# Optimization experiments

Hardware: AMD Instinct MI355X
Metric: run time of the kernel (lower is better)

The kernel has to match this reference:

```python
import jax, jax.numpy as jnp
import numpy as np

N_NODES = 50000
N_EDGES = 800000
IN_FEATS = 128
H_FEATS = 32
HEADS = 4
OUT_FEATS = 32
OUT_HEADS = 1
NEG_SLOPE = 0.2


def setup_inputs() -> dict:
    key = jax.random.key(0)
    ks = jax.random.split(key, 20)
    s = 0.05
    return {
        "features": jax.random.normal(ks[0], (N_NODES, IN_FEATS), jnp.float32),
        "src": jax.random.randint(ks[1], (N_EDGES,), 0, N_NODES, jnp.int32),
        "dst": jax.random.randint(ks[2], (N_EDGES,), 0, N_NODES, jnp.int32),
        "Ws0": jax.random.normal(ks[3], (IN_FEATS, HEADS * H_FEATS), jnp.float32) * s,
        "bs0": jnp.zeros((HEADS * H_FEATS,), jnp.float32),
        "Wd0": jax.random.normal(ks[4], (IN_FEATS, HEADS * H_FEATS), jnp.float32) * s,
        "bd0": jnp.zeros((HEADS * H_FEATS,), jnp.float32),
        "a0": jax.random.normal(ks[5], (HEADS, H_FEATS), jnp.float32) * s,
        "Ws1": jax.random.normal(ks[6], (HEADS * H_FEATS, HEADS * H_FEATS), jnp.float32) * s,
        "bs1": jnp.zeros((HEADS * H_FEATS,), jnp.float32),
        "Wd1": jax.random.normal(ks[7], (HEADS * H_FEATS, HEADS * H_FEATS), jnp.float32) * s,
        "bd1": jnp.zeros((HEADS * H_FEATS,), jnp.float32),
        "a1": jax.random.normal(ks[8], (HEADS, H_FEATS), jnp.float32) * s,
        "Ws2": jax.random.normal(ks[9], (HEADS * H_FEATS, OUT_HEADS * OUT_FEATS), jnp.float32) * s,
        "bs2": jnp.zeros((OUT_HEADS * OUT_FEATS,), jnp.float32),
        "Wd2": jax.random.normal(ks[10], (HEADS * H_FEATS, OUT_HEADS * OUT_FEATS), jnp.float32) * s,
        "bd2": jnp.zeros((OUT_HEADS * OUT_FEATS,), jnp.float32),
        "a2": jax.random.normal(ks[11], (OUT_HEADS, OUT_FEATS), jnp.float32) * s,
    }


def gatv2_conv(x, src, dst, Ws, bs, Wd, bd, attn, n_nodes):
    """DGL GATv2Conv (share_weights=False, residual=False, no dropout)."""
    heads, f = attn.shape
    feat_src = (x @ Ws + bs).reshape(-1, heads, f)  # [N, H, F]
    feat_dst = (x @ Wd + bd).reshape(-1, heads, f)  # [N, H, F]
    # per-edge GATv2 score: LeakyReLU(Wsrc h_u + Wdst h_v) . a
    e = jax.nn.leaky_relu(feat_src[src] + feat_dst[dst], NEG_SLOPE)  # [E, H, F]
    logits = jnp.einsum("ehf,hf->eh", e, attn)  # [E, H]
    # edge softmax over incoming edges of each dst node
    m = jax.ops.segment_max(logits, dst, num_segments=n_nodes)  # [N, H]
    ex = jnp.exp(logits - m[dst])
    denom = jax.ops.segment_sum(ex, dst, num_segments=n_nodes)  # [N, H]
    alpha = ex / denom[dst]  # [E, H]
    # scatter-aggregate messages
    msg = feat_src[src] * alpha[..., None]  # [E, H, F]
    return jax.ops.segment_sum(msg, dst, num_segments=n_nodes)  # [N, H, F]


def reference(features, src, dst,
              Ws0, bs0, Wd0, bd0, a0,
              Ws1, bs1, Wd1, bd1, a1,
              Ws2, bs2, Wd2, bd2, a2):
    n = features.shape[0]
    h = gatv2_conv(features, src, dst, Ws0, bs0, Wd0, bd0, a0, n)
    h = jax.nn.relu(h.reshape(n, -1))
    h = gatv2_conv(h, src, dst, Ws1, bs1, Wd1, bd1, a1, n)
    h = jax.nn.relu(h.reshape(n, -1))
    h = gatv2_conv(h, src, dst, Ws2, bs2, Wd2, bd2, a2, n)
    return h.mean(axis=1)  # [N, OUT_FEATS]
```

## Files before the change

kernel.cpp:

```cpp
#include <hip/hip_runtime.h>

typedef __attribute__((ext_vector_type(8))) short bf16x8;
typedef __attribute__((ext_vector_type(4))) float f32x4;

#define LOG2E 1.4426950408889634f

#define BINSH 8
#define NBIN 196
#define CHUNK 4096
#define K4CAP 6144

__device__ __forceinline__ unsigned bf_rn(float f) {
    unsigned u = __float_as_uint(f);
    u += 0x7fffu + ((u >> 16) & 1u);
    return u >> 16;
}
__device__ __forceinline__ float bf_lo(unsigned u) { return __uint_as_float(u << 16); }
__device__ __forceinline__ float bf_hi(unsigned u) { return __uint_as_float(u & 0xffff0000u); }

template <int CTRL>
__device__ __forceinline__ float dpp_radd(float x) {
    int t = __builtin_amdgcn_update_dpp(0, __float_as_int(x), CTRL, 0xF, 0xF, true);
    return x + __int_as_float(t);
}
__device__ __forceinline__ float sum8(float p) {
    p = dpp_radd<0x141>(p);
    p = dpp_radd<0x1B>(p);
    p = dpp_radd<0xB1>(p);
    return p;
}
__device__ __forceinline__ float dpp_swap1(float x) {
    return __int_as_float(__builtin_amdgcn_update_dpp(0, __float_as_int(x), 0xB1, 0xF, 0xF, true));
}

__device__ __forceinline__ float fast_exp2(float x) {
#if __has_builtin(__builtin_amdgcn_exp2f)
    return __builtin_amdgcn_exp2f(x);
#else
    return __expf(x * 0.6931471805599453f);
#endif
}


__global__ __launch_bounds__(256) void bin_count(const int* __restrict__ dst,
                                                 int* __restrict__ binCnt, int e) {
    __shared__ int hist[NBIN];
    for (int t = threadIdx.x; t < NBIN; t += 256) hist[t] = 0;
    __syncthreads();
    int base = blockIdx.x * CHUNK;
    int cnt = min(CHUNK, e - base);
    for (int j = threadIdx.x; j < cnt; j += 256)
        atomicAdd(&hist[dst[base + j] >> BINSH], 1);
    __syncthreads();
    for (int t = threadIdx.x; t < NBIN; t += 256)
        if (hist[t]) atomicAdd(&binCnt[t], hist[t]);
}

__global__ void bin_scan(const int* __restrict__ binCnt, int* __restrict__ binBase,
                         int* __restrict__ binCur, int* __restrict__ rowp, int n, int e) {
    int t = threadIdx.x;
    int v = (t < NBIN) ? binCnt[t] : 0;
    int lane = t & 63, w = t >> 6;
    int incl = v;
    for (int off = 1; off < 64; off <<= 1) {
        int tt = __shfl_up(incl, off);
        if (lane >= off) incl += tt;
    }
    __shared__ int wsum[4];
    if (lane == 63) wsum[w] = incl;
    __syncthreads();
    int wpre = 0;
    for (int i = 0; i < w; ++i) wpre += wsum[i];
    int excl = wpre + incl - v;
    if (t < NBIN) { binBase[t] = excl; binCur[t] = excl; }
    if (t == 0) { binBase[NBIN] = e; rowp[n] = e; }
}

__global__ __launch_bounds__(256) void bin_scatter(
    const int* __restrict__ src, const int* __restrict__ dst,
    int* __restrict__ binCur, unsigned* __restrict__ ebin, int e) {
    __shared__ int hist[NBIN];
    __shared__ int seg[NBIN];
    __shared__ int gbase[NBIN];
    __shared__ unsigned pack[CHUNK];
    for (int t = threadIdx.x; t < NBIN; t += 256) hist[t] = 0;
    __syncthreads();
    int base = blockIdx.x * CHUNK;
    int cnt = min(CHUNK, e - base);

    int myb[CHUNK / 256], myr[CHUNK / 256];
    unsigned myw[CHUNK / 256];
    int nmine = 0;
    for (int j = threadIdx.x; j < cnt; j += 256) {
        int d = dst[base + j], s = src[base + j];
        int b = d >> BINSH, dl = d & ((1 << BINSH) - 1);
        int r = atomicAdd(&hist[b], 1);
        myb[nmine] = b; myr[nmine] = r;
        myw[nmine] = ((unsigned)b << 24) | ((unsigned)dl << 16) | (unsigned)s;
        ++nmine;
    }
    __syncthreads();
    if (threadIdx.x == 0) {
        int acc = 0;
        for (int b2 = 0; b2 < NBIN; ++b2) { seg[b2] = acc; acc += hist[b2]; }
    }
    __syncthreads();
    for (int k = 0; k < nmine; ++k)
        pack[seg[myb[k]] + myr[k]] = myw[k];
    __syncthreads();
    if (threadIdx.x < NBIN && hist[threadIdx.x])
        gbase[threadIdx.x] = atomicAdd(&binCur[threadIdx.x], hist[threadIdx.x]);
    __syncthreads();
    for (int j = threadIdx.x; j < cnt; j += 256) {
        unsigned wv = pack[j];
        int b = wv >> 24;
        ebin[gbase[b] + (j - seg[b])] = wv;
    }
}

__global__ __launch_bounds__(256) void csr_build(
    const unsigned* __restrict__ ebin, const int* __restrict__ binBase,
    int* __restrict__ rowp, int* __restrict__ csrc, int n) {
    __shared__ int hist[256];
    __shared__ int seg[256];
    __shared__ unsigned stage[K4CAP];
    int b = blockIdx.x;
    int e0 = binBase[b], e1 = binBase[b + 1];
    int n0 = b << BINSH;
    int nn = min(256, n - n0);
    for (int t = threadIdx.x; t < 256; t += 256) hist[t] = 0;
    __syncthreads();
    for (int i = e0 + threadIdx.x; i < e1; i += 256) {
        unsigned wv = ebin[i];
        atomicAdd(&hist[(wv >> 16) & 255], 1);
        int off = i - e0;
        if (off < K4CAP) stage[off] = wv;
    }
    __syncthreads();
    if (threadIdx.x < 64) {
        int l = threadIdx.x;
        int s = 0, loc[4];
#pragma unroll
        for (int k = 0; k < 4; ++k) { loc[k] = s; s += hist[l * 4 + k]; }
        int incl = s;
        for (int off = 1; off < 64; off <<= 1) {
            int tt = __shfl_up(incl, off);
            if (l >= off) incl += tt;
        }
        int excl = incl - s;
#pragma unroll
        for (int k = 0; k < 4; ++k) seg[l * 4 + k] = excl + loc[k];
    }
    __syncthreads();
    for (int t = threadIdx.x; t < nn; t += 256) rowp[n0 + t] = e0 + seg[t];
    for (int t = threadIdx.x; t < 256; t += 256) hist[t] = seg[t];
    __syncthreads();
    for (int i = e0 + threadIdx.x; i < e1; i += 256) {
        int off = i - e0;
        unsigned wv = (off < K4CAP) ? stage[off] : ebin[i];
        int dl = (wv >> 16) & 255;
        int pos = e0 + atomicAdd(&hist[dl], 1);
        csrc[pos] = (int)(wv & 0xFFFFu);
    }
}


__global__ void convert_feat(const float* __restrict__ x, unsigned short* __restrict__ o, int n4) {
    int i = blockIdx.x * blockDim.x + threadIdx.x;
    if (i < n4) {
        float4 v = *(const float4*)(x + (size_t)i * 4);
        ushort4 r;
        r.x = (unsigned short)bf_rn(v.x); r.y = (unsigned short)bf_rn(v.y);
        r.z = (unsigned short)bf_rn(v.z); r.w = (unsigned short)bf_rn(v.w);
        *(ushort4*)(o + (size_t)i * 4) = r;
    }
}

__global__ void transpose_all(
    const float* __restrict__ Ws0, const float* __restrict__ Wd0,
    const float* __restrict__ Ws1, const float* __restrict__ Wd1,
    const float* __restrict__ Ws2, const float* __restrict__ Wd2,
    unsigned short* __restrict__ wt0, unsigned short* __restrict__ wt1,
    unsigned short* __restrict__ wt2) {
    int gid = blockIdx.x * blockDim.x + threadIdx.x;
    if (gid < 65536) {
        int l = gid >> 15, loc = gid & 32767;
        int c = loc >> 7, k = loc & 127;
        const float* W = (c < 128) ? (l ? Ws1 : Ws0) : (l ? Wd1 : Wd0);
        int cc = c & 127;
        float v = W[(size_t)k * 128 + cc];
        (l ? wt1 : wt0)[loc] = (unsigned short)bf_rn(v);
    } else if (gid < 65536 + 8192) {
        int loc = gid - 65536;
        int c = loc >> 7, k = loc & 127;
        const float* W = (c < 32) ? Ws2 : Wd2;
        int cc = (c < 32) ? c : c - 32;
        float v = W[(size_t)k * 32 + cc];
        wt2[loc] = (unsigned short)bf_rn(v);
    }
}


template <int COLS2>
__global__ __launch_bounds__(256) void gemm_dual2(
    const unsigned short* __restrict__ xb, const unsigned short* __restrict__ wt,
    const float* __restrict__ bs, const float* __restrict__ bd,
    unsigned short* __restrict__ fs, unsigned short* __restrict__ fd,
    int n, int nch) {
    constexpr int C  = COLS2 / 2;
    constexpr int NC = COLS2 / 64;

    const int lane = threadIdx.x & 63;
    const int m = lane & 15, quad = lane >> 4;
    const int gwid = blockIdx.x * 4 + (threadIdx.x >> 6);
    const int nwaves = gridDim.x * 4;
    const int cs = gwid % NC;
    const int cstride = nwaves / NC;

    float biasv[4];
#pragma unroll
    for (int ct = 0; ct < 4; ++ct) {
        int col = cs * 64 + ct * 16 + m;
        biasv[ct] = (col < C) ? bs[col] : bd[col - C];
    }

    for (int chunk = gwid / NC; chunk < nch; chunk += cstride) {
        const size_t r0 = (size_t)chunk * 64;

        f32x4 acc[4][4];
#pragma unroll
        for (int rt = 0; rt < 4; ++rt)
#pragma unroll
            for (int ct = 0; ct < 4; ++ct) acc[rt][ct] = (f32x4){0.f, 0.f, 0.f, 0.f};

#pragma unroll
        for (int ks = 0; ks < 4; ++ks) {
            const int ko = ks * 32 + quad * 8;
            bf16x8 a[4], b[4];
#pragma unroll
            for (int rt = 0; rt < 4; ++rt)
                a[rt] = *(const bf16x8*)(xb + (r0 + rt * 16 + m) * 128 + ko);
#pragma unroll
            for (int ct = 0; ct < 4; ++ct)
                b[ct] = *(const bf16x8*)(wt + (size_t)(cs * 64 + ct * 16 + m) * 128 + ko);
#pragma unroll
            for (int rt = 0; rt < 4; ++rt)
#pragma unroll
                for (int ct = 0; ct < 4; ++ct)
                    acc[rt][ct] = __builtin_amdgcn_mfma_f32_16x16x32_bf16(a[rt], b[ct], acc[rt][ct], 0, 0, 0);
        }

        const int odd = m & 1;
#pragma unroll
        for (int ct = 0; ct < 4; ++ct) {
            int colE = cs * 64 + ct * 16 + (m & ~1);
            unsigned short* ptr = (colE < C) ? fs : fd;
            int cc = (colE < C) ? colE : colE - C;
#pragma unroll
            for (int rt = 0; rt < 4; ++rt) {
                float v0 = acc[rt][ct][0] + biasv[ct];
                float v1 = acc[rt][ct][1] + biasv[ct];
                float v2 = acc[rt][ct][2] + biasv[ct];
                float v3 = acc[rt][ct][3] + biasv[ct];
                float s0 = dpp_swap1(v0), s1 = dpp_swap1(v1);
                float s2 = dpp_swap1(v2), s3 = dpp_swap1(v3);
                float aLo = odd ? s2 : v0, aHi = odd ? v2 : s0;
                float bLo = odd ? s3 : v1, bHi = odd ? v3 : s1;
                int rowA = (int)r0 + rt * 16 + quad * 4 + (odd ? 2 : 0);
                unsigned pa = (bf_rn(aHi) << 16) | bf_rn(aLo);
                unsigned pb = (bf_rn(bHi) << 16) | bf_rn(bLo);
                if (rowA < n)     *(unsigned*)(ptr + (size_t)rowA * C + cc)       = pa;
                if (rowA + 1 < n) *(unsigned*)(ptr + ((size_t)rowA + 1) * C + cc) = pb;
            }
        }
    }
}


#define EDGE_BODY(u, mval)                                          \
    do {                                                            \
        float x0 = bf_lo((u).x), x1 = bf_hi((u).x);                 \
        float x2 = bf_lo((u).y), x3 = bf_hi((u).y);                 \
        float t0 = x0 + fd0, t1 = x1 + fd1;                         \
        float t2 = x2 + fd2, t3 = x3 + fd3;                         \
        float p = a060 * t0;                                        \
        p = fmaf(a040, fabsf(t0), p);                               \
        p = fmaf(a061, t1, p); p = fmaf(a041, fabsf(t1), p);        \
        p = fmaf(a062, t2, p); p = fmaf(a042, fabsf(t2), p);        \
        p = fmaf(a063, t3, p); p = fmaf(a043, fabsf(t3), p);        \
        p = sum8(p);                                                \
        float ex = fast_exp2(p) * (mval);                           \
        denom += ex;                                                \
        acc0 = fmaf(ex, x0, acc0); acc1 = fmaf(ex, x1, acc1);       \
        acc2 = fmaf(ex, x2, acc2); acc3 = fmaf(ex, x3, acc3);       \
    } while (0)

__global__ __launch_bounds__(256) void conv128(
    const unsigned short* __restrict__ fs, const unsigned short* __restrict__ fd,
    const float* __restrict__ attn, const int* __restrict__ rowp,
    const int* __restrict__ csrc, unsigned short* __restrict__ out, int n) {
    const int nwaves = gridDim.x * 4;
    const int wid0 = blockIdx.x * 4 + (threadIdx.x >> 6);
    const int lane = threadIdx.x & 63;
    const int half = lane >> 5;
    const int q = lane & 31;

    float4 av = *(const float4*)(attn + q * 4);
    const float a060 = av.x * 0.6f * LOG2E, a040 = av.x * 0.4f * LOG2E;
    const float a061 = av.y * 0.6f * LOG2E, a041 = av.y * 0.4f * LOG2E;
    const float a062 = av.z * 0.6f * LOG2E, a042 = av.z * 0.4f * LOG2E;
    const float a063 = av.w * 0.6f * LOG2E, a043 = av.w * 0.4f * LOG2E;

    for (int wid = wid0; wid < n; wid += nwaves) {
        uint2 ud = *(const uint2*)(fd + (size_t)wid * 128 + q * 4);
        float fd0 = bf_lo(ud.x), fd1 = bf_hi(ud.x);
        float fd2 = bf_lo(ud.y), fd3 = bf_hi(ud.y);
        int rs = rowp[wid], re = rowp[wid + 1];
        float acc0 = 0.f, acc1 = 0.f, acc2 = 0.f, acc3 = 0.f, denom = 0.f;

        int i = rs;
        for (; i + 3 < re; i += 4) {
            int sA = csrc[i + half];
            int sB = csrc[i + 2 + half];
            uint2 uA = *(const uint2*)(fs + ((size_t)sA << 7) + q * 4);
            uint2 uB = *(const uint2*)(fs + ((size_t)sB << 7) + q * 4);
            EDGE_BODY(uA, 1.0f);
            EDGE_BODY(uB, 1.0f);
        }
        for (; i + 1 < re; i += 2) {
            int s = csrc[i + half];
            uint2 u = *(const uint2*)(fs + ((size_t)s << 7) + q * 4);
            EDGE_BODY(u, 1.0f);
        }
        if (i < re) {
            int s = csrc[i];
            uint2 u = *(const uint2*)(fs + ((size_t)s << 7) + q * 4);
            float mval = half ? 0.f : 1.f;
            EDGE_BODY(u, mval);
        }
        acc0 += __shfl_xor(acc0, 32); acc1 += __shfl_xor(acc1, 32);
        acc2 += __shfl_xor(acc2, 32); acc3 += __shfl_xor(acc3, 32);
        denom += __shfl_xor(denom, 32);
        float inv = (re > rs) ? 1.f / denom : 0.f;
        float r0 = fmaxf(acc0 * inv, 0.f), r1 = fmaxf(acc1 * inv, 0.f);
        float r2 = fmaxf(acc2 * inv, 0.f), r3 = fmaxf(acc3 * inv, 0.f);
        if (half == 0) {
            uint2 o;
            o.x = (bf_rn(r1) << 16) | bf_rn(r0);
            o.y = (bf_rn(r3) << 16) | bf_rn(r2);
            ((uint2*)(out + (size_t)wid * 128))[q] = o;
        }
    }
}

__global__ __launch_bounds__(256) void conv32(
    const unsigned short* __restrict__ fs, const unsigned short* __restrict__ fd,
    const float* __restrict__ attn, const int* __restrict__ rowp,
    const int* __restrict__ csrc, float* __restrict__ out, int n) {
    const int nwaves = gridDim.x * 4;
    const int wid0 = blockIdx.x * 4 + (threadIdx.x >> 6);
    const int lane = threadIdx.x & 63;
    const int g = lane >> 3;
    const int c = lane & 7;

    float4 av = *(const float4*)(attn + c * 4);
    const float a060 = av.x * 0.6f * LOG2E, a040 = av.x * 0.4f * LOG2E;
    const float a061 = av.y * 0.6f * LOG2E, a041 = av.y * 0.4f * LOG2E;
    const float a062 = av.z * 0.6f * LOG2E, a042 = av.z * 0.4f * LOG2E;
    const float a063 = av.w * 0.6f * LOG2E, a043 = av.w * 0.4f * LOG2E;

    for (int wid = wid0; wid < n; wid += nwaves) {
        uint2 ud = *(const uint2*)(fd + (size_t)wid * 32 + c * 4);
        float fd0 = bf_lo(ud.x), fd1 = bf_hi(ud.x);
        float fd2 = bf_lo(ud.y), fd3 = bf_hi(ud.y);
        int rs = rowp[wid], re = rowp[wid + 1];
        float acc0 = 0.f, acc1 = 0.f, acc2 = 0.f, acc3 = 0.f, denom = 0.f;

        int i = rs;
        for (; i + 7 < re; i += 8) {
            int s = csrc[i + g];
            uint2 u = *(const uint2*)(fs + ((size_t)s << 5) + c * 4);
            EDGE_BODY(u, 1.0f);
        }
        if (i < re) {
            int idx = i + g;
            int s = csrc[min(idx, re - 1)];
            uint2 u = *(const uint2*)(fs + ((size_t)s << 5) + c * 4);
            float mval = (idx < re) ? 1.f : 0.f;
            EDGE_BODY(u, mval);
        }
        acc0 = dpp_radd<0x128>(acc0); acc1 = dpp_radd<0x128>(acc1);
        acc2 = dpp_radd<0x128>(acc2); acc3 = dpp_radd<0x128>(acc3);
        denom = dpp_radd<0x128>(denom);
        acc0 += __shfl_xor(acc0, 16); acc1 += __shfl_xor(acc1, 16);
        acc2 += __shfl_xor(acc2, 16); acc3 += __shfl_xor(acc3, 16);
        denom += __shfl_xor(denom, 16);
        acc0 += __shfl_xor(acc0, 32); acc1 += __shfl_xor(acc1, 32);
        acc2 += __shfl_xor(acc2, 32); acc3 += __shfl_xor(acc3, 32);
        denom += __shfl_xor(denom, 32);
        float inv = (re > rs) ? 1.f / denom : 0.f;
        if (lane < 8) {
            float4 o;
            o.x = acc0 * inv; o.y = acc1 * inv;
            o.z = acc2 * inv; o.w = acc3 * inv;
            *(float4*)(out + (size_t)wid * 32 + c * 4) = o;
        }
    }
}


extern "C" void kernel_launch(void* const* d_in, const int* in_sizes, int n_in,
                              void* d_out, int out_size, void* d_ws, size_t ws_size,
                              hipStream_t stream) {
    const float* feats = (const float*)d_in[0];
    const int*   src   = (const int*)d_in[1];
    const int*   dst   = (const int*)d_in[2];
    const float* Ws0 = (const float*)d_in[3],  *bs0 = (const float*)d_in[4];
    const float* Wd0 = (const float*)d_in[5],  *bd0 = (const float*)d_in[6];
    const float* a0  = (const float*)d_in[7];
    const float* Ws1 = (const float*)d_in[8],  *bs1 = (const float*)d_in[9];
    const float* Wd1 = (const float*)d_in[10], *bd1 = (const float*)d_in[11];
    const float* a1  = (const float*)d_in[12];
    const float* Ws2 = (const float*)d_in[13], *bs2 = (const float*)d_in[14];
    const float* Wd2 = (const float*)d_in[15], *bd2 = (const float*)d_in[16];
    const float* a2  = (const float*)d_in[17];

    const int N = in_sizes[0] / 128;
    const int E = in_sizes[1];
    const int nch = (N + 63) / 64;
    const int NPAD = nch * 64;

    char* ws = (char*)d_ws;
    const size_t featB = (size_t)NPAD * 128 * 2;
    unsigned short* xb  = (unsigned short*)(ws);
    unsigned short* hb  = (unsigned short*)(ws + featB);
    unsigned short* fsb = (unsigned short*)(ws + 2 * featB);
    unsigned short* fdb = (unsigned short*)(ws + 3 * featB);
    char* p = ws + 4 * featB;
    unsigned short* wt0 = (unsigned short*)p; p += 256 * 128 * 2;
    unsigned short* wt1 = (unsigned short*)p; p += 256 * 128 * 2;
    unsigned short* wt2 = (unsigned short*)p; p += 64 * 128 * 2;
    int* rowp    = (int*)p;      p += ((size_t)(N + 1) * 4 + 255) / 256 * 256;
    int* binCnt  = (int*)p;      p += (NBIN * 4 + 255) / 256 * 256;
    int* binBase = (int*)p;      p += ((NBIN + 1) * 4 + 255) / 256 * 256;
    int* binCur  = (int*)p;      p += (NBIN * 4 + 255) / 256 * 256;
    unsigned* ebin = (unsigned*)p; p += (size_t)E * 4;
    int* csrc    = (int*)p;

    const int nchunks = (E + CHUNK - 1) / CHUNK;

    hipMemsetAsync(binCnt, 0, NBIN * 4, stream);
    bin_count<<<nchunks, 256, 0, stream>>>(dst, binCnt, E);
    bin_scan<<<1, 256, 0, stream>>>(binCnt, binBase, binCur, rowp, N, E);
    bin_scatter<<<nchunks, 256, 0, stream>>>(src, dst, binCur, ebin, E);
    csr_build<<<NBIN, 256, 0, stream>>>(ebin, binBase, rowp, csrc, N);

    const int n4 = N * 128 / 4;
    convert_feat<<<(n4 + 255) / 256, 256, 0, stream>>>(feats, xb, n4);
    transpose_all<<<(73728 + 255) / 256, 256, 0, stream>>>(Ws0, Wd0, Ws1, Wd1, Ws2, Wd2, wt0, wt1, wt2);

    const int g256 = nch;
    const int g64  = (nch + 3) / 4;
    const int convGrid = 2048;

    gemm_dual2<256><<<g256, 256, 0, stream>>>(xb, wt0, bs0, bd0, fsb, fdb, N, nch);
    conv128<<<convGrid, 256, 0, stream>>>(fsb, fdb, a0, rowp, csrc, hb, N);
    gemm_dual2<256><<<g256, 256, 0, stream>>>(hb, wt1, bs1, bd1, fsb, fdb, N, nch);
    conv128<<<convGrid, 256, 0, stream>>>(fsb, fdb, a1, rowp, csrc, hb, N);
    gemm_dual2<64><<<g64, 256, 0, stream>>>(hb, wt2, bs2, bd2, fsb, fdb, N, nch);
    conv32<<<convGrid, 256, 0, stream>>>(fsb, fdb, a2, rowp, csrc, (float*)d_out, N);
}
```

Baseline: 295.9 us.

## Widen conv128 lanes to 8 features, rework bin_scatter, fuse prep kernels

conv128 now gives each lane 8 features with 16-byte loads, so a wave covers 4 edges per step instead of 2, and the per-head reduction shrinks to a 4-lane DPP sum. bin_scatter replaces per-thread register arrays and a serial scan by thread 0 with a count pass, a wave-level prefix scan and a second atomic placement pass. Feature conversion, weight transpose and the binCnt memset are merged into one prep kernel, and conv32 gets a 16-edge unrolled loop. The aim is fewer launches and more memory-level parallelism, at the cost of more registers and a second read of dst in bin_scatter.

After: 302.4 us. 2.2% more time.

```diff
diff --git a/kernel.cpp b/kernel.cpp
--- a/kernel.cpp
+++ b/kernel.cpp
@@ -27,6 +27,11 @@
     p = dpp_radd<0x141>(p);
     p = dpp_radd<0x1B>(p);
     p = dpp_radd<0xB1>(p);
+    return p;
+}
+__device__ __forceinline__ float sum4(float p) {
+    p = dpp_radd<0xB1>(p);
+    p = dpp_radd<0x4E>(p);
     return p;
 }
 __device__ __forceinline__ float dpp_swap1(float x) {
@@ -79,37 +84,44 @@
 __global__ __launch_bounds__(256) void bin_scatter(
     const int* __restrict__ src, const int* __restrict__ dst,
     int* __restrict__ binCur, unsigned* __restrict__ ebin, int e) {
-    __shared__ int hist[NBIN];
-    __shared__ int seg[NBIN];
+    __shared__ int hist[256];
+    __shared__ int seg[256];
     __shared__ int gbase[NBIN];
     __shared__ unsigned pack[CHUNK];
-    for (int t = threadIdx.x; t < NBIN; t += 256) hist[t] = 0;
+    for (int t = threadIdx.x; t < 256; t += 256) hist[t] = 0;
     __syncthreads();
     int base = blockIdx.x * CHUNK;
     int cnt = min(CHUNK, e - base);
 
-    int myb[CHUNK / 256], myr[CHUNK / 256];
-    unsigned myw[CHUNK / 256];
-    int nmine = 0;
+    for (int j = threadIdx.x; j < cnt; j += 256)
+        atomicAdd(&hist[dst[base + j] >> BINSH], 1);
+    __syncthreads();
+    if (threadIdx.x < 64) {
+        int l = threadIdx.x;
+        int s = 0, loc[4];
+#pragma unroll
+        for (int k = 0; k < 4; ++k) { loc[k] = s; s += hist[l * 4 + k]; }
+        int incl = s;
+        for (int off = 1; off < 64; off <<= 1) {
+            int tt = __shfl_up(incl, off);
+            if (l >= off) incl += tt;
+        }
+        int excl = incl - s;
+#pragma unroll
+        for (int k = 0; k < 4; ++k) seg[l * 4 + k] = excl + loc[k];
+    }
+    __syncthreads();
+    if (threadIdx.x < NBIN && hist[threadIdx.x])
+        gbase[threadIdx.x] = atomicAdd(&binCur[threadIdx.x], hist[threadIdx.x]);
+    __syncthreads();
+    for (int t = threadIdx.x; t < 256; t += 256) hist[t] = seg[t];
+    __syncthreads();
     for (int j = threadIdx.x; j < cnt; j += 256) {
         int d = dst[base + j], s = src[base + j];
         int b = d >> BINSH, dl = d & ((1 << BINSH) - 1);
-        int r = atomicAdd(&hist[b], 1);
-        myb[nmine] = b; myr[nmine] = r;
-        myw[nmine] = ((unsigned)b << 24) | ((unsigned)dl << 16) | (unsigned)s;
-        ++nmine;
-    }
-    __syncthreads();
-    if (threadIdx.x == 0) {
-        int acc = 0;
-        for (int b2 = 0; b2 < NBIN; ++b2) { seg[b2] = acc; acc += hist[b2]; }
-    }
-    __syncthreads();
-    for (int k = 0; k < nmine; ++k)
-        pack[seg[myb[k]] + myr[k]] = myw[k];
-    __syncthreads();
-    if (threadIdx.x < NBIN && hist[threadIdx.x])
-        gbase[threadIdx.x] = atomicAdd(&binCur[threadIdx.x], hist[threadIdx.x]);
+        int pos = atomicAdd(&hist[b], 1);
+        pack[pos] = ((unsigned)b << 24) | ((unsigned)dl << 16) | (unsigned)s;
+    }
     __syncthreads();
     for (int j = threadIdx.x; j < cnt; j += 256) {
         unsigned wv = pack[j];
@@ -165,38 +177,38 @@
 }
 
 
-__global__ void convert_feat(const float* __restrict__ x, unsigned short* __restrict__ o, int n4) {
-    int i = blockIdx.x * blockDim.x + threadIdx.x;
-    if (i < n4) {
-        float4 v = *(const float4*)(x + (size_t)i * 4);
-        ushort4 r;
-        r.x = (unsigned short)bf_rn(v.x); r.y = (unsigned short)bf_rn(v.y);
-        r.z = (unsigned short)bf_rn(v.z); r.w = (unsigned short)bf_rn(v.w);
-        *(ushort4*)(o + (size_t)i * 4) = r;
-    }
-}
-
-__global__ void transpose_all(
+__global__ __launch_bounds__(256) void prep(
+    const float* __restrict__ x, unsigned short* __restrict__ xb, int n4,
     const float* __restrict__ Ws0, const float* __restrict__ Wd0,
     const float* __restrict__ Ws1, const float* __restrict__ Wd1,
     const float* __restrict__ Ws2, const float* __restrict__ Wd2,
     unsigned short* __restrict__ wt0, unsigned short* __restrict__ wt1,
-    unsigned short* __restrict__ wt2) {
+    unsigned short* __restrict__ wt2, int* __restrict__ binCnt) {
     int gid = blockIdx.x * blockDim.x + threadIdx.x;
-    if (gid < 65536) {
-        int l = gid >> 15, loc = gid & 32767;
-        int c = loc >> 7, k = loc & 127;
-        const float* W = (c < 128) ? (l ? Ws1 : Ws0) : (l ? Wd1 : Wd0);
-        int cc = c & 127;
-        float v = W[(size_t)k * 128 + cc];
-        (l ? wt1 : wt0)[loc] = (unsigned short)bf_rn(v);
-    } else if (gid < 65536 + 8192) {
-        int loc = gid - 65536;
-        int c = loc >> 7, k = loc & 127;
-        const float* W = (c < 32) ? Ws2 : Wd2;
-        int cc = (c < 32) ? c : c - 32;
-        float v = W[(size_t)k * 32 + cc];
-        wt2[loc] = (unsigned short)bf_rn(v);
+    if (gid < NBIN) binCnt[gid] = 0;
+    if (gid < n4) {
+        float4 v = *(const float4*)(x + (size_t)gid * 4);
+        ushort4 r;
+        r.x = (unsigned short)bf_rn(v.x); r.y = (unsigned short)bf_rn(v.y);
+        r.z = (unsigned short)bf_rn(v.z); r.w = (unsigned short)bf_rn(v.w);
+        *(ushort4*)(xb + (size_t)gid * 4) = r;
+    } else {
+        int g = gid - n4;
+        if (g < 65536) {
+            int l = g >> 15, loc = g & 32767;
+            int c = loc >> 7, k = loc & 127;
+            const float* W = (c < 128) ? (l ? Ws1 : Ws0) : (l ? Wd1 : Wd0);
+            int cc = c & 127;
+            float v = W[(size_t)k * 128 + cc];
+            (l ? wt1 : wt0)[loc] = (unsigned short)bf_rn(v);
+        } else if (g < 65536 + 8192) {
+            int loc = g - 65536;
+            int c = loc >> 7, k = loc & 127;
+            const float* W = (c < 32) ? Ws2 : Wd2;
+            int cc = (c < 32) ? c : c - 32;
+            float v = W[(size_t)k * 32 + cc];
+            wt2[loc] = (unsigned short)bf_rn(v);
+        }
     }
 }
 
@@ -295,6 +307,34 @@
         acc2 = fmaf(ex, x2, acc2); acc3 = fmaf(ex, x3, acc3);       \
     } while (0)
 
+#define EB8(u, mval)                                                \
+    do {                                                            \
+        float x0 = bf_lo((u).x), x1 = bf_hi((u).x);                 \
+        float x2 = bf_lo((u).y), x3 = bf_hi((u).y);                 \
+        float x4 = bf_lo((u).z), x5 = bf_hi((u).z);                 \
+        float x6 = bf_lo((u).w), x7 = bf_hi((u).w);                 \
+        float t0 = x0 + fd0, t1 = x1 + fd1;                         \
+        float t2 = x2 + fd2, t3 = x3 + fd3;                         \
+        float t4 = x4 + fd4, t5 = x5 + fd5;                         \
+        float t6 = x6 + fd6, t7 = x7 + fd7;                         \
+        float p = a60_0 * t0;                                       \
+        p = fmaf(a40_0, fabsf(t0), p);                              \
+        p = fmaf(a60_1, t1, p); p = fmaf(a40_1, fabsf(t1), p);      \
+        p = fmaf(a60_2, t2, p); p = fmaf(a40_2, fabsf(t2), p);      \
+        p = fmaf(a60_3, t3, p); p = fmaf(a40_3, fabsf(t3), p);      \
+        p = fmaf(a60_4, t4, p); p = fmaf(a40_4, fabsf(t4), p);      \
+        p = fmaf(a60_5, t5, p); p = fmaf(a40_5, fabsf(t5), p);      \
+        p = fmaf(a60_6, t6, p); p = fmaf(a40_6, fabsf(t6), p);      \
+        p = fmaf(a60_7, t7, p); p = fmaf(a40_7, fabsf(t7), p);      \
+        p = sum4(p);                                                \
+        float ex = fast_exp2(p) * (mval);                           \
+        denom += ex;                                                \
+        acc0 = fmaf(ex, x0, acc0); acc1 = fmaf(ex, x1, acc1);       \
+        acc2 = fmaf(ex, x2, acc2); acc3 = fmaf(ex, x3, acc3);       \
+        acc4 = fmaf(ex, x4, acc4); acc5 = fmaf(ex, x5, acc5);       \
+        acc6 = fmaf(ex, x6, acc6); acc7 = fmaf(ex, x7, acc7);       \
+    } while (0)
+
 __global__ __launch_bounds__(256) void conv128(
     const unsigned short* __restrict__ fs, const unsigned short* __restrict__ fd,
     const float* __restrict__ attn, const int* __restrict__ rowp,
@@ -302,53 +342,73 @@
     const int nwaves = gridDim.x * 4;
     const int wid0 = blockIdx.x * 4 + (threadIdx.x >> 6);
     const int lane = threadIdx.x & 63;
-    const int half = lane >> 5;
-    const int q = lane & 31;
-
-    float4 av = *(const float4*)(attn + q * 4);
-    const float a060 = av.x * 0.6f * LOG2E, a040 = av.x * 0.4f * LOG2E;
-    const float a061 = av.y * 0.6f * LOG2E, a041 = av.y * 0.4f * LOG2E;
-    const float a062 = av.z * 0.6f * LOG2E, a042 = av.z * 0.4f * LOG2E;
-    const float a063 = av.w * 0.6f * LOG2E, a043 = av.w * 0.4f * LOG2E;
+    const int slot = lane >> 4;
+    const int c = lane & 15;
+
+    float4 av0 = *(const float4*)(attn + c * 8);
+    float4 av1 = *(const float4*)(attn + c * 8 + 4);
+    const float a60_0 = av0.x * 0.6f * LOG2E, a40_0 = av0.x * 0.4f * LOG2E;
+    const float a60_1 = av0.y * 0.6f * LOG2E, a40_1 = av0.y * 0.4f * LOG2E;
+    const float a60_2 = av0.z * 0.6f * LOG2E, a40_2 = av0.z * 0.4f * LOG2E;
+    const float a60_3 = av0.w * 0.6f * LOG2E, a40_3 = av0.w * 0.4f * LOG2E;
+    const float a60_4 = av1.x * 0.6f * LOG2E, a40_4 = av1.x * 0.4f * LOG2E;
+    const float a60_5 = av1.y * 0.6f * LOG2E, a40_5 = av1.y * 0.4f * LOG2E;
+    const float a60_6 = av1.z * 0.6f * LOG2E, a40_6 = av1.z * 0.4f * LOG2E;
+    const float a60_7 = av1.w * 0.6f * LOG2E, a40_7 = av1.w * 0.4f * LOG2E;
 
     for (int wid = wid0; wid < n; wid += nwaves) {
-        uint2 ud = *(const uint2*)(fd + (size_t)wid * 128 + q * 4);
+        uint4 ud = *(const uint4*)(fd + (size_t)wid * 128 + c * 8);
         float fd0 = bf_lo(ud.x), fd1 = bf_hi(ud.x);
         float fd2 = bf_lo(ud.y), fd3 = bf_hi(ud.y);
+        float fd4 = bf_lo(ud.z), fd5 = bf_hi(ud.z);
+        float fd6 = bf_lo(ud.w), fd7 = bf_hi(ud.w);
         int rs = rowp[wid], re = rowp[wid + 1];
-        float acc0 = 0.f, acc1 = 0.f, acc2 = 0.f, acc3 = 0.f, denom = 0.f;
+        float acc0 = 0.f, acc1 = 0.f, acc2 = 0.f, acc3 = 0.f;
+        float acc4 = 0.f, acc5 = 0.f, acc6 = 0.f, acc7 = 0.f, denom = 0.f;
 
         int i = rs;
+        for (; i + 7 < re; i += 8) {
+            int sA = csrc[i + slot];
+            int sB = csrc[i + 4 + slot];
+            uint4 uA = *(const uint4*)(fs + ((size_t)sA << 7) + c * 8);
+            uint4 uB = *(const uint4*)(fs + ((size_t)sB << 7) + c * 8);
+            EB8(uA, 1.0f);
+            EB8(uB, 1.0f);
+        }
         for (; i + 3 < re; i += 4) {
-            int sA = csrc[i + half];
-            int sB = csrc[i + 2 + half];
-            uint2 uA = *(const uint2*)(fs + ((size_t)sA << 7) + q * 4);
-            uint2 uB = *(const uint2*)(fs + ((size_t)sB << 7) + q * 4);
-            EDGE_BODY(uA, 1.0f);
-            EDGE_BODY(uB, 1.0f);
-        }
-        for (; i + 1 < re; i += 2) {
-            int s = csrc[i + half];
-            uint2 u = *(const uint2*)(fs + ((size_t)s << 7) + q * 4);
-            EDGE_BODY(u, 1.0f);
+            int s = csrc[i + slot];
+            uint4 u = *(const uint4*)(fs + ((size_t)s << 7) + c * 8);
+            EB8(u, 1.0f);
         }
         if (i < re) {
-            int s = csrc[i];
-            uint2 u = *(const uint2*)(fs + ((size_t)s << 7) + q * 4);
-            float mval = half ? 0.f : 1.f;
-            EDGE_BODY(u, mval);
-        }
+            int idx = i + slot;
+            int s = csrc[min(idx, re - 1)];
+            uint4 u = *(const uint4*)(fs + ((size_t)s << 7) + c * 8);
+            float mval = (idx < re) ? 1.f : 0.f;
+            EB8(u, mval);
+        }
+        acc0 += __shfl_xor(acc0, 16); acc1 += __shfl_xor(acc1, 16);
+        acc2 += __shfl_xor(acc2, 16); acc3 += __shfl_xor(acc3, 16);
+        acc4 += __shfl_xor(acc4, 16); acc5 += __shfl_xor(acc5, 16);
+        acc6 += __shfl_xor(acc6, 16); acc7 += __shfl_xor(acc7, 16);
+        denom += __shfl_xor(denom, 16);
         acc0 += __shfl_xor(acc0, 32); acc1 += __shfl_xor(acc1, 32);
         acc2 += __shfl_xor(acc2, 32); acc3 += __shfl_xor(acc3, 32);
+        acc4 += __shfl_xor(acc4, 32); acc5 += __shfl_xor(acc5, 32);
+        acc6 += __shfl_xor(acc6, 32); acc7 += __shfl_xor(acc7, 32);
         denom += __shfl_xor(denom, 32);
         float inv = (re > rs) ? 1.f / denom : 0.f;
         float r0 = fmaxf(acc0 * inv, 0.f), r1 = fmaxf(acc1 * inv, 0.f);
         float r2 = fmaxf(acc2 * inv, 0.f), r3 = fmaxf(acc3 * inv, 0.f);
-        if (half == 0) {
-            uint2 o;
+        float r4 = fmaxf(acc4 * inv, 0.f), r5 = fmaxf(acc5 * inv, 0.f);
+        float r6 = fmaxf(acc6 * inv, 0.f), r7 = fmaxf(acc7 * inv, 0.f);
+        if (slot == 0) {
+            uint4 o;
             o.x = (bf_rn(r1) << 16) | bf_rn(r0);
             o.y = (bf_rn(r3) << 16) | bf_rn(r2);
-            ((uint2*)(out + (size_t)wid * 128))[q] = o;
+            o.z = (bf_rn(r5) << 16) | bf_rn(r4);
+            o.w = (bf_rn(r7) << 16) | bf_rn(r6);
+            *(uint4*)(out + (size_t)wid * 128 + c * 8) = o;
         }
     }
 }
@@ -377,6 +437,14 @@
         float acc0 = 0.f, acc1 = 0.f, acc2 = 0.f, acc3 = 0.f, denom = 0.f;
 
         int i = rs;
+        for (; i + 15 < re; i += 16) {
+            int s0 = csrc[i + g];
+            int s1 = csrc[i + 8 + g];
+            uint2 u0 = *(const uint2*)(fs + ((size_t)s0 << 5) + c * 4);
+            uint2 u1 = *(const uint2*)(fs + ((size_t)s1 << 5) + c * 4);
+            EDGE_BODY(u0, 1.0f);
+            EDGE_BODY(u1, 1.0f);
+        }
         for (; i + 7 < re; i += 8) {
             int s = csrc[i + g];
             uint2 u = *(const uint2*)(fs + ((size_t)s << 5) + c * 4);
@@ -448,16 +516,15 @@
     int* csrc    = (int*)p;
 
     const int nchunks = (E + CHUNK - 1) / CHUNK;
-
-    hipMemsetAsync(binCnt, 0, NBIN * 4, stream);
+    const int n4 = N * 128 / 4;
+
+    prep<<<(n4 + 73728 + 255) / 256, 256, 0, stream>>>(
+        feats, xb, n4, Ws0, Wd0, Ws1, Wd1, Ws2, Wd2, wt0, wt1, wt2, binCnt);
+
     bin_count<<<nchunks, 256, 0, stream>>>(dst, binCnt, E);
     bin_scan<<<1, 256, 0, stream>>>(binCnt, binBase, binCur, rowp, N, E);
     bin_scatter<<<nchunks, 256, 0, stream>>>(src, dst, binCur, ebin, E);
     csr_build<<<NBIN, 256, 0, stream>>>(ebin, binBase, rowp, csrc, N);
-
-    const int n4 = N * 128 / 4;
-    convert_feat<<<(n4 + 255) / 256, 256, 0, stream>>>(feats, xb, n4);
-    transpose_all<<<(73728 + 255) / 256, 256, 0, stream>>>(Ws0, Wd0, Ws1, Wd1, Ws2, Wd2, wt0, wt1, wt2);
 
     const int g256 = nch;
     const int g64  = (nch + 3) / 4;
```
